# Kernel optimization log

Hardware: AMD Instinct MI355X
Metric: run time of the kernel (lower is better)

## Reference

```python
import jax, jax.numpy as jnp
import numpy as np
from jax import lax

H = 64           # hid_size (hard-pinned by reshape(4,6,64) in source)
B = 16384        # number of months (prototype batch)
A = 16           # agent_num
N = B * A        # rows of `inputs`
P = 24           # num_prototypes = 4 * 6
T = 32           # jieqi_info sequence length
ACT = 12         # action_dim
EPS = 1e-4       # self.epsilon
BN_EPS = 1e-5
LN_EPS = 1e-5


def _lstm_step(h, c, x, w_ih, w_hh, b_ih, b_hh):
    # torch LSTM gate order: i, f, g, o
    g = x @ w_ih.T + h @ w_hh.T + b_ih + b_hh
    i, f, gg, o = jnp.split(g, 4, axis=-1)
    c = jax.nn.sigmoid(f) * c + jax.nn.sigmoid(i) * jnp.tanh(gg)
    h = jax.nn.sigmoid(o) * jnp.tanh(c)
    return h, c


def setup_inputs() -> dict:
    key = jax.random.key(0)
    ks = iter(jax.random.split(key, 40))

    def nrm(shape, s=0.05):
        return jax.random.normal(next(ks), shape, jnp.float32) * s

    inp = {
        "inputs": jax.random.normal(next(ks), (N, H), jnp.float32),
        "hidden_state": jax.random.normal(next(ks), (N, H), jnp.float32),
        "month": jax.random.randint(next(ks), (B,), 0, 12, jnp.int32),
        "jieqi_info": jax.random.normal(next(ks), (P, T, 3), jnp.float32),
        # bidirectional LSTM (input 3 -> hidden H), forward + backward dirs
        "w_ih_f": nrm((4 * H, 3)), "w_hh_f": nrm((4 * H, H)),
        "b_ih_f": nrm((4 * H,)), "b_hh_f": nrm((4 * H,)),
        "w_ih_b": nrm((4 * H, 3)), "w_hh_b": nrm((4 * H, H)),
        "b_ih_b": nrm((4 * H,)), "b_hh_b": nrm((4 * H,)),
        "fcl_w": nrm((H, 2 * H)), "fcl_b": nrm((H,)),      # jieqi_lstm_fc
        "proj_w": nrm((H, H)),                               # proto_proj (no bias)
        "conv_w": nrm((H, 2 * H)), "conv_b": nrm((H,)),    # conv_global
        "bn_g": jnp.ones((H,), jnp.float32), "bn_b": jnp.zeros((H,), jnp.float32),
        "fc1_w": nrm((H, H)), "fc1_b": nrm((H,)),
        "ln_g": jnp.ones((H,), jnp.float32), "ln_b": jnp.zeros((H,), jnp.float32),
        "gru_wih": nrm((3 * H, H)), "gru_whh": nrm((3 * H, H)),
        "gru_bih": nrm((3 * H,)), "gru_bhh": nrm((3 * H,)),
        "out_w": nrm((ACT, H)), "out_b": nrm((ACT,)),
    }
    # last_layer weight: +1 on correct class, -0.5 on incorrect (set_last_layer_incorrect_connection)
    ident = np.zeros((P, 4), np.float32)
    ident[np.arange(P), np.arange(P) // 6] = 1.0
    inp["last_w"] = jnp.asarray(1.0 * ident.T + (-0.5) * (1.0 - ident.T))  # [4, 24]
    return inp


def reference(inputs, hidden_state, month, jieqi_info,
              w_ih_f, w_hh_f, b_ih_f, b_hh_f,
              w_ih_b, w_hh_b, b_ih_b, b_hh_b,
              fcl_w, fcl_b, proj_w, last_w,
              conv_w, conv_b, bn_g, bn_b,
              fc1_w, fc1_b, ln_g, ln_b,
              gru_wih, gru_whh, gru_bih, gru_bhh,
              out_w, out_b):
    dt = inputs.dtype
    # ---- get_jieqi_prototype: biLSTM over [P, T, 3], take output at t=T-1 ----
    z0 = jnp.zeros((P, H), dt)

    def step(carry, x_t):
        h, c = carry
        h, c = _lstm_step(h, c, x_t, w_ih_f, w_hh_f, b_ih_f, b_hh_f)
        return (h, c), None

    (h_f, _), _ = lax.scan(step, (z0, z0), jnp.swapaxes(jieqi_info, 0, 1))
    # backward direction's output at the last time index = one step on x[:, -1]
    h_b, _ = _lstm_step(z0, z0, jieqi_info[:, -1, :], w_ih_b, w_hh_b, b_ih_b, b_hh_b)
    th = jnp.concatenate([h_f, h_b], axis=-1)                 # [P, 2H]
    pv = jax.nn.relu(th @ fcl_w.T + fcl_b) @ proj_w.T         # prototype_vectors [P, H]

    # ---- prototype_distances on full input batch ----
    xp = inputs @ pv.T                                        # [N, P]
    min_distances = (-2.0 * xp
                     + jnp.sum(inputs ** 2, axis=1, keepdims=True)
                     + jnp.sum(pv ** 2, axis=1)[None, :])
    prototype_activations = jnp.log((min_distances + 1.0) / (min_distances + EPS))
    logits = prototype_activations @ last_w.T                 # [N, 4]

    # ---- month -> season, select seasonal prototype block ----
    seasons = jnp.mod(jnp.floor_divide(month - 2, 3), 4)      # 2-4:0, 5-7:1, 8-10:2, else 3
    sub_proto = pv.reshape(4, 6, H)[seasons]                  # [B, 6, H]

    # ---- prototype_subgraph_distances (vectorized over the 6 protos) ----
    xr = inputs.reshape(B, A, H)
    d = jnp.sum((xr[:, None, :, :] - sub_proto[:, :, None, :]) ** 2, axis=-1)  # [B, 6, A]
    sim = jnp.mean(jnp.log((d + 1.0) / (d + EPS)), axis=2)    # [B, 6]

    # ---- argmax + gather + repeat ----
    chosen_idx = jnp.argmax(sim, axis=1)                      # [B]
    chosen = sub_proto[jnp.arange(B), chosen_idx]             # [B, H]
    chosen = jnp.broadcast_to(chosen[:, None, :], (B, A, H)).reshape(N, H)

    # ---- conv_global -> batchnorm(train) -> relu ----
    x_glb = jnp.concatenate([inputs, chosen], axis=-1) @ conv_w.T + conv_b
    mu = jnp.mean(x_glb, axis=0)
    var = jnp.mean((x_glb - mu) ** 2, axis=0)                 # biased, training-mode BN
    x_glb = (x_glb - mu) * lax.rsqrt(var + BN_EPS) * bn_g + bn_b
    x_glb = jax.nn.relu(x_glb)

    # ---- fc1 -> layernorm -> relu ----
    x = x_glb @ fc1_w.T + fc1_b
    lmu = jnp.mean(x, axis=-1, keepdims=True)
    lvar = jnp.mean((x - lmu) ** 2, axis=-1, keepdims=True)
    x = (x - lmu) * lax.rsqrt(lvar + LN_EPS) * ln_g + ln_b
    x = jax.nn.relu(x)

    # ---- GRUCell ----
    h_in = hidden_state.reshape(-1, H)
    gi = x @ gru_wih.T + gru_bih
    gh = h_in @ gru_whh.T + gru_bhh
    r = jax.nn.sigmoid(gi[:, :H] + gh[:, :H])
    zg = jax.nn.sigmoid(gi[:, H:2 * H] + gh[:, H:2 * H])
    n = jnp.tanh(gi[:, 2 * H:] + r * gh[:, 2 * H:])
    h = (1.0 - zg) * n + zg * h_in

    a = h @ out_w.T + out_b
    return (a, h, logits, min_distances)
```

## Files before the change

kernel.cpp:

```cpp
#include <hip/hip_runtime.h>
#include <cmath>

#define NHID 64
#define NMONTH 16384
#define NAGENT 16
#define NROWS (NMONTH*NAGENT)
#define NPROTO 24
#define TSEQ 32
#define NACT 12
#define EPS_P  1e-4f
#define EPS_BN 1e-5f
#define EPS_LN 1e-5f

typedef __attribute__((ext_vector_type(8))) short short8;
typedef __attribute__((ext_vector_type(4))) float f32x4;
typedef __attribute__((ext_vector_type(4))) unsigned short us4;
typedef __attribute__((ext_vector_type(8))) unsigned short us8;
typedef unsigned short ushort_t;

#define MFMA(a,b,c) __builtin_amdgcn_mfma_f32_16x16x32_bf16(a,b,c,0,0,0)
#define LPAD 68

#define WS_TH     0
#define WS_PV     3072
#define WS_PVSQ   4608
#define WS_CTAB   4640
#define WS_MID1   6176
#define WS_MID2   14368
#define WS_BNSC   22560
#define WS_BNSH   22624
#define WS_WBF16  22688
#define WO_FC1   0
#define WO_GIH   4096
#define WO_GHH   16384
#define WO_OUT   28672
#define WO_PV    29696
#define WO_CVX   31744

__device__ __forceinline__ float sigf(float x){ return 1.0f/(1.0f+expf(-x)); }
__device__ __forceinline__ float fsig(float x){
  return __builtin_amdgcn_rcpf(1.f + __expf(-x));
}
__device__ __forceinline__ float ftanh(float x){
  return 1.f - 2.f*__builtin_amdgcn_rcpf(1.f + __expf(2.f*x));
}
__device__ __forceinline__ ushort_t f2bf(float f){
  unsigned u = __builtin_bit_cast(unsigned, f);
  u += 0x7FFFu + ((u>>16)&1u);
  return (ushort_t)(u>>16);
}
__device__ __forceinline__ float bf2f(ushort_t b){
  return __builtin_bit_cast(float, ((unsigned)b)<<16);
}

__global__ __launch_bounds__(256) void k1_lstm(
    const float* __restrict__ jq,
    const float* __restrict__ wif, const float* __restrict__ whf,
    const float* __restrict__ bif, const float* __restrict__ bhf,
    const float* __restrict__ wib, const float* __restrict__ bib, const float* __restrict__ bhb,
    float* __restrict__ th)
{
  const int p = blockIdx.x;
  const int j = threadIdx.x;
  __shared__ float hs[NHID];
  __shared__ float gs[4*NHID];
  float wh[NHID];
  #pragma unroll
  for (int k=0;k<NHID;k++) wh[k] = whf[j*NHID+k];
  const float wi0=wif[j*3], wi1=wif[j*3+1], wi2=wif[j*3+2];
  const float bj = bif[j]+bhf[j];
  float c = 0.f;
  if (j < NHID) hs[j] = 0.f;
  __syncthreads();
  for (int t=0;t<TSEQ;t++){
    const float x0=jq[(p*TSEQ+t)*3], x1=jq[(p*TSEQ+t)*3+1], x2=jq[(p*TSEQ+t)*3+2];
    float g = wi0*x0+wi1*x1+wi2*x2+bj;
    #pragma unroll
    for (int k=0;k<NHID;k++) g += wh[k]*hs[k];
    __syncthreads();
    gs[j] = g;
    __syncthreads();
    if (j < NHID){
      const float gi=gs[j], gf=gs[NHID+j], gg=gs[2*NHID+j], go=gs[3*NHID+j];
      c = sigf(gf)*c + sigf(gi)*tanhf(gg);
      hs[j] = sigf(go)*tanhf(c);
    }
    __syncthreads();
  }
  if (j < NHID) th[p*2*NHID + j] = hs[j];
  const float x0=jq[(p*TSEQ+TSEQ-1)*3], x1=jq[(p*TSEQ+TSEQ-1)*3+1], x2=jq[(p*TSEQ+TSEQ-1)*3+2];
  const float gb = wib[j*3]*x0 + wib[j*3+1]*x1 + wib[j*3+2]*x2 + bib[j]+bhb[j];
  __syncthreads();
  gs[j] = gb;
  __syncthreads();
  if (j < NHID){
    const float gi=gs[j], gg=gs[2*NHID+j], go=gs[3*NHID+j];
    const float cb = sigf(gi)*tanhf(gg);
    th[p*2*NHID + NHID + j] = sigf(go)*tanhf(cb);
  }
}

__global__ __launch_bounds__(64) void k2_proto(
    const float* __restrict__ th, const float* __restrict__ fclw, const float* __restrict__ fclb,
    const float* __restrict__ projw, const float* __restrict__ convw, const float* __restrict__ convb,
    float* __restrict__ pv, float* __restrict__ pvsq, float* __restrict__ ctab)
{
  const int p = blockIdx.x, h = threadIdx.x;
  __shared__ float thr[2*NHID], t1[NHID], pvr[NHID];
  thr[h]      = th[p*2*NHID+h];
  thr[NHID+h] = th[p*2*NHID+NHID+h];
  __syncthreads();
  float acc = fclb[h];
  for (int k=0;k<2*NHID;k++) acc += thr[k]*fclw[h*2*NHID+k];
  t1[h] = fmaxf(acc,0.f);
  __syncthreads();
  float pvh = 0.f;
  for (int k=0;k<NHID;k++) pvh += t1[k]*projw[h*NHID+k];
  pv[p*NHID+h]=pvh; pvr[h]=pvh;
  __syncthreads();
  float ct = convb[h];
  for (int k=0;k<NHID;k++) ct += pvr[k]*convw[h*2*NHID+NHID+k];
  ctab[p*NHID+h]=ct;
  if (h==0){ float s=0.f; for (int k=0;k<NHID;k++) s+=pvr[k]*pvr[k]; pvsq[p]=s; }
}

__global__ __launch_bounds__(256) void k5w_bf16(
    const float* __restrict__ fc1w, const float* __restrict__ gwih,
    const float* __restrict__ gwhh, const float* __restrict__ outw,
    const float* __restrict__ pvf, const float* __restrict__ convw,
    ushort_t* __restrict__ wb)
{
  const int t = threadIdx.x;
  for (int i=t;i<4096;i+=256)  wb[WO_FC1+i]=f2bf(fc1w[i]);
  for (int i=t;i<12288;i+=256){ wb[WO_GIH+i]=f2bf(gwih[i]); wb[WO_GHH+i]=f2bf(gwhh[i]); }
  for (int i=t;i<1024;i+=256)  wb[WO_OUT+i] = (i<768)? f2bf(outw[i]) : (ushort_t)0;
  for (int i=t;i<2048;i+=256)  wb[WO_PV+i]  = (i<1536)? f2bf(pvf[i]) : (ushort_t)0;
  for (int i=t;i<4096;i+=256)  wb[WO_CVX+i] = f2bf(convw[(i>>6)*128 + (i&63)]);
}

__global__ __launch_bounds__(256) void k3_mfma(
    const float* __restrict__ inp, const int* __restrict__ month,
    const float* __restrict__ pvsq, const float* __restrict__ ctab,
    const float* __restrict__ lastw, const ushort_t* __restrict__ wb,
    float* __restrict__ out_logits, float* __restrict__ out_md,
    ushort_t* __restrict__ xgb, float* __restrict__ part1, float* __restrict__ part2)
{
  __shared__ ushort_t xl[64*72];
  __shared__ float insql[64];
  __shared__ float pal[64*26];
  __shared__ int qs[4];

  const int t = threadIdx.x;
  const int w = t>>6, lane = t&63;
  const int l15 = lane&15, kg = lane>>4, ko = kg*8;
  const int gcol = w*16 + l15;
  const size_t rowblk = (size_t)blockIdx.x*64;

  const short8 pv0a = *reinterpret_cast<const short8*>(wb + WO_PV + l15*64 + ko);
  const short8 pv0b = *reinterpret_cast<const short8*>(wb + WO_PV + l15*64 + 32 + ko);
  const short8 pv1a = *reinterpret_cast<const short8*>(wb + WO_PV + (16+l15)*64 + ko);
  const short8 pv1b = *reinterpret_cast<const short8*>(wb + WO_PV + (16+l15)*64 + 32 + ko);
  const short8 cw0  = *reinterpret_cast<const short8*>(wb + WO_CVX + gcol*64 + ko);
  const short8 cw1  = *reinterpret_cast<const short8*>(wb + WO_CVX + gcol*64 + 32 + ko);

  {
    const int r = t>>2, cb = (t&3)*16;
    const float* xrow = inp + (rowblk + r)*64 + cb;
    float s = 0.f;
    #pragma unroll
    for (int i=0;i<4;i++){
      const float4 xv = *reinterpret_cast<const float4*>(xrow + i*4);
      s += xv.x*xv.x + xv.y*xv.y + xv.z*xv.z + xv.w*xv.w;
      us4 y; y.x=f2bf(xv.x); y.y=f2bf(xv.y); y.z=f2bf(xv.z); y.w=f2bf(xv.w);
      *reinterpret_cast<us4*>(&xl[r*72+cb+i*4]) = y;
    }
    s += __shfl_xor(s,1,4);
    s += __shfl_xor(s,2,4);
    if ((t&3)==0) insql[r] = s;
  }
  __syncthreads();

  const int rowA = w*16 + l15;
  const short8 ax0 = *reinterpret_cast<const short8*>(&xl[rowA*72+ko]);
  const short8 ax1 = *reinterpret_cast<const short8*>(&xl[rowA*72+32+ko]);

  f32x4 d0={0.f,0.f,0.f,0.f}, d1=d0;
  d0 = MFMA(ax0, pv0a, d0);
  d0 = MFMA(ax1, pv0b, d0);
  d1 = MFMA(ax0, pv1a, d1);
  d1 = MFMA(ax1, pv1b, d1);
  {
    const float pq0 = pvsq[l15];
    const float pq1 = (l15<8)? pvsq[16+l15] : 0.f;
    #pragma unroll
    for (int j=0;j<4;j++){
      const int rloc = w*16 + kg*4 + j;
      const float iq = insql[rloc];
      const float md0 = iq + pq0 - 2.f*d0[j];
      out_md[(rowblk+rloc)*24 + l15] = md0;
      pal[rloc*26 + l15] = __logf(md0+1.f) - __logf(md0+EPS_P);
      const float md1 = iq + pq1 - 2.f*d1[j];
      const float pa1 = __logf(md1+1.f) - __logf(md1+EPS_P);
      if (l15<8){
        out_md[(rowblk+rloc)*24 + 16+l15] = md1;
        pal[rloc*26 + 16+l15] = pa1;
      }
    }
  }
  __syncthreads();

  {
    const int r = t>>2, c = t&3;
    float lgv = 0.f;
    #pragma unroll
    for (int p=0;p<24;p++) lgv += pal[r*26+p]*lastw[c*24+p];
    out_logits[(rowblk+r)*4 + c] = lgv;
  }

  {
    const int mo = month[blockIdx.x*4 + w];
    const int season = ((mo+10)%12)/3;
    float simv = -3.4e38f;
    const int j6 = lane & 7;
    if (j6 < 6){
      simv = 0.f;
      const int sp = season*6 + j6;
      #pragma unroll
      for (int i=0;i<16;i++) simv += pal[(w*16+i)*26 + sp];
    }
    int bidx = j6;
    { const float ov=__shfl_xor(simv,1,8); const int oi=__shfl_xor(bidx,1,8);
      if (ov>simv || (ov==simv && oi<bidx)){ simv=ov; bidx=oi; } }
    { const float ov=__shfl_xor(simv,2,8); const int oi=__shfl_xor(bidx,2,8);
      if (ov>simv || (ov==simv && oi<bidx)){ simv=ov; bidx=oi; } }
    { const float ov=__shfl_xor(simv,4,8); const int oi=__shfl_xor(bidx,4,8);
      if (ov>simv || (ov==simv && oi<bidx)){ simv=ov; bidx=oi; } }
    if (lane==0) qs[w] = season*6 + bidx;
  }
  __syncthreads();

  ushort_t* xgblk = xgb + (size_t)blockIdx.x*8192;
  float s1=0.f, s2=0.f;
  #pragma unroll
  for (int rg=0; rg<4; rg++){
    const int ra = rg*16 + l15;
    const short8 bx0 = *reinterpret_cast<const short8*>(&xl[ra*72+ko]);
    const short8 bx1 = *reinterpret_cast<const short8*>(&xl[ra*72+32+ko]);
    f32x4 ac={0.f,0.f,0.f,0.f};
    ac = MFMA(bx0, cw0, ac);
    ac = MFMA(bx1, cw1, ac);
    const float cg = ctab[qs[rg]*64 + gcol];
    #pragma unroll
    for (int j=0;j<4;j++){
      const int rloc = rg*16 + kg*4 + j;
      const float v = ac[j] + cg;
      xgblk[rloc*64 + gcol] = f2bf(v);
      s1 += v; s2 += v*v;
    }
  }
  s1 += __shfl_xor(s1,16); s1 += __shfl_xor(s1,32);
  s2 += __shfl_xor(s2,16); s2 += __shfl_xor(s2,32);
  if (kg==0){
    part1[blockIdx.x*64 + gcol] = s1;
    part2[blockIdx.x*64 + gcol] = s2;
  }
}

__global__ __launch_bounds__(64) void k4b_reduce(
    const float* __restrict__ part1, const float* __restrict__ part2,
    double* __restrict__ mid1, double* __restrict__ mid2)
{
  const int i = blockIdx.x, c = threadIdx.x;
  double s1=0.0, s2=0.0;
  for (int b=i*64; b<i*64+64; b++){
    s1 += (double)part1[b*64+c];
    s2 += (double)part2[b*64+c];
  }
  mid1[i*64+c]=s1; mid2[i*64+c]=s2;
}

__global__ __launch_bounds__(64) void k5_finalize(
    const double* __restrict__ mid1, const double* __restrict__ mid2,
    const float* __restrict__ bng, const float* __restrict__ bnb,
    float* __restrict__ bnsc, float* __restrict__ bnsh)
{
  const int f = threadIdx.x;
  double s1=0.0, s2=0.0;
  for (int i=0;i<64;i++){ s1+=mid1[i*64+f]; s2+=mid2[i*64+f]; }
  const double mu = s1 / (double)NROWS;
  double var = s2/(double)NROWS - mu*mu;
  if (var < 0.0) var = 0.0;
  const float sc = bng[f] * (float)(1.0/sqrt(var + (double)EPS_BN));
  bnsc[f]=sc;
  bnsh[f]=bnb[f]-(float)mu*sc;
}

__global__ __launch_bounds__(256) void k6_mfma(
    const ushort_t* __restrict__ xgb, const float* __restrict__ hidden,
    const float* __restrict__ bnsc, const float* __restrict__ bnsh,
    const float* __restrict__ fc1b, const float* __restrict__ lng, const float* __restrict__ lnb,
    const float* __restrict__ gbih, const float* __restrict__ gbhh,
    const float* __restrict__ outb,
    const ushort_t* __restrict__ wb,
    float* __restrict__ out_a, float* __restrict__ out_h)
{
  __shared__ ushort_t ybuf[64*LPAD];
  __shared__ ushort_t hidl[64*LPAD];
  const int t = threadIdx.x;
  const int lane = t & 63, w = t >> 6;
  const int l15 = lane & 15, kg = lane >> 4;
  const int ko = kg*8;

  const short8 f0a = *reinterpret_cast<const short8*>(wb + WO_FC1 + ( 0+l15)*64 + ko);
  const short8 f0b = *reinterpret_cast<const short8*>(wb + WO_FC1 + ( 0+l15)*64 + 32 + ko);
  const short8 f1a = *reinterpret_cast<const short8*>(wb + WO_FC1 + (16+l15)*64 + ko);
  const short8 f1b = *reinterpret_cast<const short8*>(wb + WO_FC1 + (16+l15)*64 + 32 + ko);
  const short8 f2a = *reinterpret_cast<const short8*>(wb + WO_FC1 + (32+l15)*64 + ko);
  const short8 f2b = *reinterpret_cast<const short8*>(wb + WO_FC1 + (32+l15)*64 + 32 + ko);
  const short8 f3a = *reinterpret_cast<const short8*>(wb + WO_FC1 + (48+l15)*64 + ko);
  const short8 f3b = *reinterpret_cast<const short8*>(wb + WO_FC1 + (48+l15)*64 + 32 + ko);

  {
    const int r = t>>2, cb = (t&3)*16;
    const ushort_t* xgp = xgb + (size_t)blockIdx.x*8192 + r*64 + cb;
    const us8 xv0 = *reinterpret_cast<const us8*>(xgp);
    const us8 xv1 = *reinterpret_cast<const us8*>(xgp+8);
    float xf[16];
    #pragma unroll
    for (int e=0;e<8;e++){ xf[e]=bf2f(xv0[e]); xf[8+e]=bf2f(xv1[e]); }
    const size_t g = ((size_t)blockIdx.x*64 + r)*64 + cb;
    #pragma unroll
    for (int i=0;i<4;i++){
      const float4 sc = *reinterpret_cast<const float4*>(bnsc + cb + i*4);
      const float4 sh = *reinterpret_cast<const float4*>(bnsh + cb + i*4);
      us4 y;
      y.x = f2bf(fmaxf(xf[4*i  ]*sc.x+sh.x,0.f));
      y.y = f2bf(fmaxf(xf[4*i+1]*sc.y+sh.y,0.f));
      y.z = f2bf(fmaxf(xf[4*i+2]*sc.z+sh.z,0.f));
      y.w = f2bf(fmaxf(xf[4*i+3]*sc.w+sh.w,0.f));
      *reinterpret_cast<us4*>(&ybuf[r*LPAD + cb + i*4]) = y;
      const float4 hv4 = *reinterpret_cast<const float4*>(hidden + g + i*4);
      us4 hb;
      hb.x=f2bf(hv4.x); hb.y=f2bf(hv4.y); hb.z=f2bf(hv4.z); hb.w=f2bf(hv4.w);
      *reinterpret_cast<us4*>(&hidl[r*LPAD + cb + i*4]) = hb;
    }
  }
  __syncthreads();

  const int rowA = w*16 + l15;
  const short8 ay0 = *reinterpret_cast<const short8*>(&ybuf[rowA*LPAD + ko]);
  const short8 ay1 = *reinterpret_cast<const short8*>(&ybuf[rowA*LPAD + 32 + ko]);

  f32x4 ac0={0.f,0.f,0.f,0.f}, ac1=ac0, ac2=ac0, ac3=ac0;
  ac0 = MFMA(ay0, f0a, ac0);  ac0 = MFMA(ay1, f0b, ac0);
  ac1 = MFMA(ay0, f1a, ac1);  ac1 = MFMA(ay1, f1b, ac1);
  ac2 = MFMA(ay0, f2a, ac2);  ac2 = MFMA(ay1, f2b, ac2);
  ac3 = MFMA(ay0, f3a, ac3);  ac3 = MFMA(ay1, f3b, ac3);
  {
    const float b0=fc1b[l15], b1=fc1b[16+l15], b2=fc1b[32+l15], b3=fc1b[48+l15];
    float tn0[4], tn1[4], tn2[4], tn3[4], mu[4], rs[4];
    #pragma unroll
    for (int j=0;j<4;j++){ tn0[j]=ac0[j]+b0; tn1[j]=ac1[j]+b1; tn2[j]=ac2[j]+b2; tn3[j]=ac3[j]+b3; }
    #pragma unroll
    for (int j=0;j<4;j++){
      float s = tn0[j]+tn1[j]+tn2[j]+tn3[j];
      s += __shfl_xor(s,1,16); s += __shfl_xor(s,2,16);
      s += __shfl_xor(s,4,16); s += __shfl_xor(s,8,16);
      mu[j] = s*(1.f/64.f);
    }
    #pragma unroll
    for (int j=0;j<4;j++){
      const float d0_=tn0[j]-mu[j], d1_=tn1[j]-mu[j], d2_=tn2[j]-mu[j], d3_=tn3[j]-mu[j];
      float v = d0_*d0_+d1_*d1_+d2_*d2_+d3_*d3_;
      v += __shfl_xor(v,1,16); v += __shfl_xor(v,2,16);
      v += __shfl_xor(v,4,16); v += __shfl_xor(v,8,16);
      rs[j] = 1.f/sqrtf(v*(1.f/64.f)+EPS_LN);
    }
    const float g0=lng[l15], g1=lng[16+l15], g2=lng[32+l15], g3=lng[48+l15];
    const float q0=lnb[l15], q1=lnb[16+l15], q2=lnb[32+l15], q3=lnb[48+l15];
    #pragma unroll
    for (int j=0;j<4;j++){
      const int rr_ = w*16 + kg*4 + j;
      ybuf[rr_*LPAD +      l15] = f2bf(fmaxf((tn0[j]-mu[j])*rs[j]*g0+q0, 0.f));
      ybuf[rr_*LPAD + 16 + l15] = f2bf(fmaxf((tn1[j]-mu[j])*rs[j]*g1+q1, 0.f));
      ybuf[rr_*LPAD + 32 + l15] = f2bf(fmaxf((tn2[j]-mu[j])*rs[j]*g2+q2, 0.f));
      ybuf[rr_*LPAD + 48 + l15] = f2bf(fmaxf((tn3[j]-mu[j])*rs[j]*g3+q3, 0.f));
    }
  }

  const int gcol = w*16 + l15;
  const ushort_t* gih = wb + WO_GIH;
  const ushort_t* ghh = wb + WO_GHH;
  const short8 wr0 = *reinterpret_cast<const short8*>(gih + (      gcol)*64 + ko);
  const short8 wr1 = *reinterpret_cast<const short8*>(gih + (      gcol)*64 + 32 + ko);
  const short8 wz0 = *reinterpret_cast<const short8*>(gih + ( 64 + gcol)*64 + ko);
  const short8 wz1 = *reinterpret_cast<const short8*>(gih + ( 64 + gcol)*64 + 32 + ko);
  const short8 wn0 = *reinterpret_cast<const short8*>(gih + (128 + gcol)*64 + ko);
  const short8 wn1 = *reinterpret_cast<const short8*>(gih + (128 + gcol)*64 + 32 + ko);
  const short8 vr0 = *reinterpret_cast<const short8*>(ghh + (      gcol)*64 + ko);
  const short8 vr1 = *reinterpret_cast<const short8*>(ghh + (      gcol)*64 + 32 + ko);
  const short8 vz0 = *reinterpret_cast<const short8*>(ghh + ( 64 + gcol)*64 + ko);
  const short8 vz1 = *reinterpret_cast<const short8*>(ghh + ( 64 + gcol)*64 + 32 + ko);
  const short8 vn0 = *reinterpret_cast<const short8*>(ghh + (128 + gcol)*64 + ko);
  const short8 vn1 = *reinterpret_cast<const short8*>(ghh + (128 + gcol)*64 + 32 + ko);
  const float bir=gbih[gcol],     bhr=gbhh[gcol];
  const float biz=gbih[64+gcol],  bhz=gbhh[64+gcol];
  const float bin_=gbih[128+gcol],bhn=gbhh[128+gcol];
  __syncthreads();

  us4 hkeep[4];
  #pragma unroll
  for (int rg=0; rg<4; rg++){
    const int ra = rg*16 + l15;
    const short8 at0 = *reinterpret_cast<const short8*>(&ybuf[ra*LPAD + ko]);
    const short8 at1 = *reinterpret_cast<const short8*>(&ybuf[ra*LPAD + 32 + ko]);
    const short8 bh0 = *reinterpret_cast<const short8*>(&hidl[ra*LPAD + ko]);
    const short8 bh1 = *reinterpret_cast<const short8*>(&hidl[ra*LPAD + 32 + ko]);
    f32x4 ar={0.f,0.f,0.f,0.f}, az=ar, an=ar, hn=ar;
    ar = MFMA(at0, wr0, ar);  ar = MFMA(at1, wr1, ar);
    ar = MFMA(bh0, vr0, ar);  ar = MFMA(bh1, vr1, ar);
    az = MFMA(at0, wz0, az);  az = MFMA(at1, wz1, az);
    az = MFMA(bh0, vz0, az);  az = MFMA(bh1, vz1, az);
    an = MFMA(at0, wn0, an);  an = MFMA(at1, wn1, an);
    hn = MFMA(bh0, vn0, hn);  hn = MFMA(bh1, vn1, hn);
    us4 hb4;
    #pragma unroll
    for (int j=0;j<4;j++){
      const int rloc = rg*16 + kg*4 + j;
      const size_t rg_ = (size_t)blockIdx.x*64 + rloc;
      const float rrg = fsig(ar[j]+bir+bhr);
      const float zzg = fsig(az[j]+biz+bhz);
      const float nng = ftanh(an[j]+bin_ + rrg*(hn[j]+bhn));
      const float hold = bf2f(hidl[rloc*LPAD + gcol]);
      const float hv = (1.f-zzg)*nng + zzg*hold;
      out_h[rg_*64 + gcol] = hv;
      hb4[j] = f2bf(hv);
    }
    hkeep[rg] = hb4;
  }

  const short8 ow0 = *reinterpret_cast<const short8*>(wb + WO_OUT + l15*64 + ko);
  const short8 ow1 = *reinterpret_cast<const short8*>(wb + WO_OUT + l15*64 + 32 + ko);
  const float ob = (l15 < 12) ? outb[l15] : 0.f;

  __syncthreads();
  #pragma unroll
  for (int rg=0; rg<4; rg++){
    #pragma unroll
    for (int j=0;j<4;j++)
      ybuf[(rg*16 + kg*4 + j)*LPAD + gcol] = hkeep[rg][j];
  }
  __syncthreads();

  const short8 av0 = *reinterpret_cast<const short8*>(&ybuf[rowA*LPAD + ko]);
  const short8 av1 = *reinterpret_cast<const short8*>(&ybuf[rowA*LPAD + 32 + ko]);
  f32x4 aa={0.f,0.f,0.f,0.f};
  aa = MFMA(av0, ow0, aa);
  aa = MFMA(av1, ow1, aa);
  if (l15 < 12){
    #pragma unroll
    for (int j=0;j<4;j++){
      const size_t rg_ = (size_t)blockIdx.x*64 + w*16 + kg*4 + j;
      out_a[rg_*12 + l15] = aa[j] + ob;
    }
  }
}

extern "C" void kernel_launch(void* const* d_in, const int* in_sizes, int n_in,
                              void* d_out, int out_size, void* d_ws, size_t ws_size,
                              hipStream_t stream)
{
  (void)in_sizes; (void)n_in; (void)out_size; (void)ws_size;
  const float* inputs = (const float*)d_in[0];
  const float* hidden = (const float*)d_in[1];
  const int*   month  = (const int*)d_in[2];
  const float* jq     = (const float*)d_in[3];
  const float* wif    = (const float*)d_in[4];
  const float* whf    = (const float*)d_in[5];
  const float* bif    = (const float*)d_in[6];
  const float* bhf    = (const float*)d_in[7];
  const float* wib    = (const float*)d_in[8];
  const float* bib    = (const float*)d_in[10];
  const float* bhb    = (const float*)d_in[11];
  const float* fclw   = (const float*)d_in[12];
  const float* fclb   = (const float*)d_in[13];
  const float* projw  = (const float*)d_in[14];
  const float* convw  = (const float*)d_in[15];
  const float* convb  = (const float*)d_in[16];
  const float* bng    = (const float*)d_in[17];
  const float* bnb    = (const float*)d_in[18];
  const float* fc1w   = (const float*)d_in[19];
  const float* fc1b   = (const float*)d_in[20];
  const float* lng    = (const float*)d_in[21];
  const float* lnb    = (const float*)d_in[22];
  const float* gwih   = (const float*)d_in[23];
  const float* gwhh   = (const float*)d_in[24];
  const float* gbih   = (const float*)d_in[25];
  const float* gbhh   = (const float*)d_in[26];
  const float* outw   = (const float*)d_in[27];
  const float* outb   = (const float*)d_in[28];
  const float* lastw  = (const float*)d_in[29];

  float* ws  = (float*)d_ws;
  float* out = (float*)d_out;
  float* out_a  = out;
  float* out_h  = out + (size_t)NROWS*NACT;
  float* out_lg = out + (size_t)NROWS*(NACT+NHID);
  float* out_md = out + (size_t)NROWS*(NACT+NHID+4);
  ushort_t* wb = (ushort_t*)(ws + WS_WBF16);
  ushort_t* xgb = (ushort_t*)out_h;
  float* part1 = out_a;
  float* part2 = out_a + 4096*64;

  hipLaunchKernelGGL(k1_lstm, dim3(NPROTO), dim3(256), 0, stream,
                     jq, wif, whf, bif, bhf, wib, bib, bhb, ws+WS_TH);
  hipLaunchKernelGGL(k2_proto, dim3(NPROTO), dim3(64), 0, stream,
                     ws+WS_TH, fclw, fclb, projw, convw, convb,
                     ws+WS_PV, ws+WS_PVSQ, ws+WS_CTAB);
  hipLaunchKernelGGL(k5w_bf16, dim3(1), dim3(256), 0, stream,
                     fc1w, gwih, gwhh, outw, ws+WS_PV, convw, wb);
  hipLaunchKernelGGL(k3_mfma, dim3(NROWS/64), dim3(256), 0, stream,
                     inputs, month, ws+WS_PVSQ, ws+WS_CTAB, lastw, wb,
                     out_lg, out_md, xgb, part1, part2);
  hipLaunchKernelGGL(k4b_reduce, dim3(64), dim3(64), 0, stream,
                     part1, part2, (double*)(ws+WS_MID1), (double*)(ws+WS_MID2));
  hipLaunchKernelGGL(k5_finalize, dim3(1), dim3(64), 0, stream,
                     (const double*)(ws+WS_MID1), (const double*)(ws+WS_MID2),
                     bng, bnb, ws+WS_BNSC, ws+WS_BNSH);
  hipLaunchKernelGGL(k6_mfma, dim3(NROWS/64), dim3(256), 0, stream,
                     xgb, hidden, ws+WS_BNSC, ws+WS_BNSH, fc1b, lng, lnb,
                     gbih, gbhh, outb, wb, out_a, out_h);
}
```

Measured before the change: 161.1 us.

## Make each wave own its rows to replace block barriers with wave-local fences

In k3_mfma and k6_mfma the work split changes so each wave owns 16 rows across all 64 output columns, instead of 16 columns across all 64 rows. Because every value a wave reads from shared memory is now written by that same wave, the block-wide __syncthreads calls become an LDS waitcnt fence, and the qs shared array and the hkeep staging for the output matmul go away. The cost is that the conv and GRU weight fragments are loaded inside the per-column-tile loop, roughly four times more weight loads per wave. The BN partial sums are also written per wave, four times as many, so k4b_reduce reads four times more partials and their offsets grow accordingly.

```diff
diff --git a/kernel.cpp b/kernel.cpp
--- a/kernel.cpp
+++ b/kernel.cpp
@@ -20,6 +20,7 @@
 
 #define MFMA(a,b,c) __builtin_amdgcn_mfma_f32_16x16x32_bf16(a,b,c,0,0,0)
 #define LPAD 68
+#define LDSFENCE() asm volatile("s_waitcnt lgkmcnt(0)" ::: "memory")
 
 #define WS_TH     0
 #define WS_PV     3072
@@ -148,23 +149,22 @@
   __shared__ ushort_t xl[64*72];
   __shared__ float insql[64];
   __shared__ float pal[64*26];
-  __shared__ int qs[4];
 
   const int t = threadIdx.x;
   const int w = t>>6, lane = t&63;
   const int l15 = lane&15, kg = lane>>4, ko = kg*8;
-  const int gcol = w*16 + l15;
+  const int rbase = w*16;
   const size_t rowblk = (size_t)blockIdx.x*64;
 
   const short8 pv0a = *reinterpret_cast<const short8*>(wb + WO_PV + l15*64 + ko);
   const short8 pv0b = *reinterpret_cast<const short8*>(wb + WO_PV + l15*64 + 32 + ko);
   const short8 pv1a = *reinterpret_cast<const short8*>(wb + WO_PV + (16+l15)*64 + ko);
   const short8 pv1b = *reinterpret_cast<const short8*>(wb + WO_PV + (16+l15)*64 + 32 + ko);
-  const short8 cw0  = *reinterpret_cast<const short8*>(wb + WO_CVX + gcol*64 + ko);
-  const short8 cw1  = *reinterpret_cast<const short8*>(wb + WO_CVX + gcol*64 + 32 + ko);
+  const int mo = month[blockIdx.x*4 + w];
+  const int season = ((mo+10)%12)/3;
 
   {
-    const int r = t>>2, cb = (t&3)*16;
+    const int r = rbase + (lane>>2), cb = (lane&3)*16;
     const float* xrow = inp + (rowblk + r)*64 + cb;
     float s = 0.f;
     #pragma unroll
@@ -176,11 +176,11 @@
     }
     s += __shfl_xor(s,1,4);
     s += __shfl_xor(s,2,4);
-    if ((t&3)==0) insql[r] = s;
-  }
-  __syncthreads();
-
-  const int rowA = w*16 + l15;
+    if ((lane&3)==0) insql[r] = s;
+  }
+  LDSFENCE();
+
+  const int rowA = rbase + l15;
   const short8 ax0 = *reinterpret_cast<const short8*>(&xl[rowA*72+ko]);
   const short8 ax1 = *reinterpret_cast<const short8*>(&xl[rowA*72+32+ko]);
 
@@ -194,7 +194,7 @@
     const float pq1 = (l15<8)? pvsq[16+l15] : 0.f;
     #pragma unroll
     for (int j=0;j<4;j++){
-      const int rloc = w*16 + kg*4 + j;
+      const int rloc = rbase + kg*4 + j;
       const float iq = insql[rloc];
       const float md0 = iq + pq0 - 2.f*d0[j];
       out_md[(rowblk+rloc)*24 + l15] = md0;
@@ -207,26 +207,25 @@
       }
     }
   }
-  __syncthreads();
+  LDSFENCE();
 
   {
-    const int r = t>>2, c = t&3;
+    const int r2 = rbase + (lane>>2), c = lane&3;
     float lgv = 0.f;
     #pragma unroll
-    for (int p=0;p<24;p++) lgv += pal[r*26+p]*lastw[c*24+p];
-    out_logits[(rowblk+r)*4 + c] = lgv;
-  }
-
+    for (int p=0;p<24;p++) lgv += pal[r2*26+p]*lastw[c*24+p];
+    out_logits[(rowblk+r2)*4 + c] = lgv;
+  }
+
+  int qsw;
   {
-    const int mo = month[blockIdx.x*4 + w];
-    const int season = ((mo+10)%12)/3;
     float simv = -3.4e38f;
     const int j6 = lane & 7;
     if (j6 < 6){
       simv = 0.f;
       const int sp = season*6 + j6;
       #pragma unroll
-      for (int i=0;i<16;i++) simv += pal[(w*16+i)*26 + sp];
+      for (int i=0;i<16;i++) simv += pal[(rbase+i)*26 + sp];
     }
     int bidx = j6;
     { const float ov=__shfl_xor(simv,1,8); const int oi=__shfl_xor(bidx,1,8);
@@ -235,34 +234,33 @@
       if (ov>simv || (ov==simv && oi<bidx)){ simv=ov; bidx=oi; } }
     { const float ov=__shfl_xor(simv,4,8); const int oi=__shfl_xor(bidx,4,8);
       if (ov>simv || (ov==simv && oi<bidx)){ simv=ov; bidx=oi; } }
-    if (lane==0) qs[w] = season*6 + bidx;
-  }
-  __syncthreads();
+    qsw = season*6 + bidx;
+  }
 
   ushort_t* xgblk = xgb + (size_t)blockIdx.x*8192;
-  float s1=0.f, s2=0.f;
   #pragma unroll
-  for (int rg=0; rg<4; rg++){
-    const int ra = rg*16 + l15;
-    const short8 bx0 = *reinterpret_cast<const short8*>(&xl[ra*72+ko]);
-    const short8 bx1 = *reinterpret_cast<const short8*>(&xl[ra*72+32+ko]);
+  for (int ct=0; ct<4; ct++){
+    const int c = ct*16 + l15;
+    const short8 cw0 = *reinterpret_cast<const short8*>(wb + WO_CVX + c*64 + ko);
+    const short8 cw1 = *reinterpret_cast<const short8*>(wb + WO_CVX + c*64 + 32 + ko);
     f32x4 ac={0.f,0.f,0.f,0.f};
-    ac = MFMA(bx0, cw0, ac);
-    ac = MFMA(bx1, cw1, ac);
-    const float cg = ctab[qs[rg]*64 + gcol];
-    #pragma unroll
-    for (int j=0;j<4;j++){
-      const int rloc = rg*16 + kg*4 + j;
+    ac = MFMA(ax0, cw0, ac);
+    ac = MFMA(ax1, cw1, ac);
+    const float cg = ctab[qsw*64 + c];
+    float s1=0.f, s2=0.f;
+    #pragma unroll
+    for (int j=0;j<4;j++){
+      const int rloc = rbase + kg*4 + j;
       const float v = ac[j] + cg;
-      xgblk[rloc*64 + gcol] = f2bf(v);
+      xgblk[rloc*64 + c] = f2bf(v);
       s1 += v; s2 += v*v;
     }
-  }
-  s1 += __shfl_xor(s1,16); s1 += __shfl_xor(s1,32);
-  s2 += __shfl_xor(s2,16); s2 += __shfl_xor(s2,32);
-  if (kg==0){
-    part1[blockIdx.x*64 + gcol] = s1;
-    part2[blockIdx.x*64 + gcol] = s2;
+    s1 += __shfl_xor(s1,16); s1 += __shfl_xor(s1,32);
+    s2 += __shfl_xor(s2,16); s2 += __shfl_xor(s2,32);
+    if (kg==0){
+      part1[((size_t)blockIdx.x*4 + w)*64 + c] = s1;
+      part2[((size_t)blockIdx.x*4 + w)*64 + c] = s2;
+    }
   }
 }
 
@@ -272,7 +270,7 @@
 {
   const int i = blockIdx.x, c = threadIdx.x;
   double s1=0.0, s2=0.0;
-  for (int b=i*64; b<i*64+64; b++){
+  for (int b=i*256; b<i*256+256; b++){
     s1 += (double)part1[b*64+c];
     s2 += (double)part2[b*64+c];
   }
@@ -310,6 +308,7 @@
   const int lane = t & 63, w = t >> 6;
   const int l15 = lane & 15, kg = lane >> 4;
   const int ko = kg*8;
+  const int rbase = w*16;
 
   const short8 f0a = *reinterpret_cast<const short8*>(wb + WO_FC1 + ( 0+l15)*64 + ko);
   const short8 f0b = *reinterpret_cast<const short8*>(wb + WO_FC1 + ( 0+l15)*64 + 32 + ko);
@@ -321,7 +320,7 @@
   const short8 f3b = *reinterpret_cast<const short8*>(wb + WO_FC1 + (48+l15)*64 + 32 + ko);
 
   {
-    const int r = t>>2, cb = (t&3)*16;
+    const int r = rbase + (lane>>2), cb = (lane&3)*16;
     const ushort_t* xgp = xgb + (size_t)blockIdx.x*8192 + r*64 + cb;
     const us8 xv0 = *reinterpret_cast<const us8*>(xgp);
     const us8 xv1 = *reinterpret_cast<const us8*>(xgp+8);
@@ -345,11 +344,13 @@
       *reinterpret_cast<us4*>(&hidl[r*LPAD + cb + i*4]) = hb;
     }
   }
-  __syncthreads();
-
-  const int rowA = w*16 + l15;
+  LDSFENCE();
+
+  const int rowA = rbase + l15;
   const short8 ay0 = *reinterpret_cast<const short8*>(&ybuf[rowA*LPAD + ko]);
   const short8 ay1 = *reinterpret_cast<const short8*>(&ybuf[rowA*LPAD + 32 + ko]);
+  const short8 bh0 = *reinterpret_cast<const short8*>(&hidl[rowA*LPAD + ko]);
+  const short8 bh1 = *reinterpret_cast<const short8*>(&hidl[rowA*LPAD + 32 + ko]);
 
   f32x4 ac0={0.f,0.f,0.f,0.f}, ac1=ac0, ac2=ac0, ac3=ac0;
   ac0 = MFMA(ay0, f0a, ac0);  ac0 = MFMA(ay1, f0b, ac0);
@@ -380,42 +381,39 @@
     const float q0=lnb[l15], q1=lnb[16+l15], q2=lnb[32+l15], q3=lnb[48+l15];
     #pragma unroll
     for (int j=0;j<4;j++){
-      const int rr_ = w*16 + kg*4 + j;
+      const int rr_ = rbase + kg*4 + j;
       ybuf[rr_*LPAD +      l15] = f2bf(fmaxf((tn0[j]-mu[j])*rs[j]*g0+q0, 0.f));
       ybuf[rr_*LPAD + 16 + l15] = f2bf(fmaxf((tn1[j]-mu[j])*rs[j]*g1+q1, 0.f));
       ybuf[rr_*LPAD + 32 + l15] = f2bf(fmaxf((tn2[j]-mu[j])*rs[j]*g2+q2, 0.f));
       ybuf[rr_*LPAD + 48 + l15] = f2bf(fmaxf((tn3[j]-mu[j])*rs[j]*g3+q3, 0.f));
     }
   }
-
-  const int gcol = w*16 + l15;
+  LDSFENCE();
+
+  const short8 at0 = *reinterpret_cast<const short8*>(&ybuf[rowA*LPAD + ko]);
+  const short8 at1 = *reinterpret_cast<const short8*>(&ybuf[rowA*LPAD + 32 + ko]);
+
   const ushort_t* gih = wb + WO_GIH;
   const ushort_t* ghh = wb + WO_GHH;
-  const short8 wr0 = *reinterpret_cast<const short8*>(gih + (      gcol)*64 + ko);
-  const short8 wr1 = *reinterpret_cast<const short8*>(gih + (      gcol)*64 + 32 + ko);
-  const short8 wz0 = *reinterpret_cast<const short8*>(gih + ( 64 + gcol)*64 + ko);
-  const short8 wz1 = *reinterpret_cast<const short8*>(gih + ( 64 + gcol)*64 + 32 + ko);
-  const short8 wn0 = *reinterpret_cast<const short8*>(gih + (128 + gcol)*64 + ko);
-  const short8 wn1 = *reinterpret_cast<const short8*>(gih + (128 + gcol)*64 + 32 + ko);
-  const short8 vr0 = *reinterpret_cast<const short8*>(ghh + (      gcol)*64 + ko);
-  const short8 vr1 = *reinterpret_cast<const short8*>(ghh + (      gcol)*64 + 32 + ko);
-  const short8 vz0 = *reinterpret_cast<const short8*>(ghh + ( 64 + gcol)*64 + ko);
-  const short8 vz1 = *reinterpret_cast<const short8*>(ghh + ( 64 + gcol)*64 + 32 + ko);
-  const short8 vn0 = *reinterpret_cast<const short8*>(ghh + (128 + gcol)*64 + ko);
-  const short8 vn1 = *reinterpret_cast<const short8*>(ghh + (128 + gcol)*64 + 32 + ko);
-  const float bir=gbih[gcol],     bhr=gbhh[gcol];
-  const float biz=gbih[64+gcol],  bhz=gbhh[64+gcol];
-  const float bin_=gbih[128+gcol],bhn=gbhh[128+gcol];
-  __syncthreads();
-
-  us4 hkeep[4];
   #pragma unroll
-  for (int rg=0; rg<4; rg++){
-    const int ra = rg*16 + l15;
-    const short8 at0 = *reinterpret_cast<const short8*>(&ybuf[ra*LPAD + ko]);
-    const short8 at1 = *reinterpret_cast<const short8*>(&ybuf[ra*LPAD + 32 + ko]);
-    const short8 bh0 = *reinterpret_cast<const short8*>(&hidl[ra*LPAD + ko]);
-    const short8 bh1 = *reinterpret_cast<const short8*>(&hidl[ra*LPAD + 32 + ko]);
+  for (int ct=0; ct<4; ct++){
+    const int c = ct*16 + l15;
+    const short8 wr0 = *reinterpret_cast<const short8*>(gih + (      c)*64 + ko);
+    const short8 wr1 = *reinterpret_cast<const short8*>(gih + (      c)*64 + 32 + ko);
+    const short8 wz0 = *reinterpret_cast<const short8*>(gih + ( 64 + c)*64 + ko);
+    const short8 wz1 = *reinterpret_cast<const short8*>(gih + ( 64 + c)*64 + 32 + ko);
+    const short8 wn0 = *reinterpret_cast<const short8*>(gih + (128 + c)*64 + ko);
+    const short8 wn1 = *reinterpret_cast<const short8*>(gih + (128 + c)*64 + 32 + ko);
+    const short8 vr0 = *reinterpret_cast<const short8*>(ghh + (      c)*64 + ko);
+    const short8 vr1 = *reinterpret_cast<const short8*>(ghh + (      c)*64 + 32 + ko);
+    const short8 vz0 = *reinterpret_cast<const short8*>(ghh + ( 64 + c)*64 + ko);
+    const short8 vz1 = *reinterpret_cast<const short8*>(ghh + ( 64 + c)*64 + 32 + ko);
+    const short8 vn0 = *reinterpret_cast<const short8*>(ghh + (128 + c)*64 + ko);
+    const short8 vn1 = *reinterpret_cast<const short8*>(ghh + (128 + c)*64 + 32 + ko);
+    const float br  = gbih[c]      + gbhh[c];
+    const float bz  = gbih[64+c]   + gbhh[64+c];
+    const float bn_ = gbih[128+c];
+    const float bhn = gbhh[128+c];
     f32x4 ar={0.f,0.f,0.f,0.f}, az=ar, an=ar, hn=ar;
     ar = MFMA(at0, wr0, ar);  ar = MFMA(at1, wr1, ar);
     ar = MFMA(bh0, vr0, ar);  ar = MFMA(bh1, vr1, ar);
@@ -423,34 +421,24 @@
     az = MFMA(bh0, vz0, az);  az = MFMA(bh1, vz1, az);
     an = MFMA(at0, wn0, an);  an = MFMA(at1, wn1, an);
     hn = MFMA(bh0, vn0, hn);  hn = MFMA(bh1, vn1, hn);
-    us4 hb4;
-    #pragma unroll
-    for (int j=0;j<4;j++){
-      const int rloc = rg*16 + kg*4 + j;
+    #pragma unroll
+    for (int j=0;j<4;j++){
+      const int rloc = rbase + kg*4 + j;
       const size_t rg_ = (size_t)blockIdx.x*64 + rloc;
-      const float rrg = fsig(ar[j]+bir+bhr);
-      const float zzg = fsig(az[j]+biz+bhz);
-      const float nng = ftanh(an[j]+bin_ + rrg*(hn[j]+bhn));
-      const float hold = bf2f(hidl[rloc*LPAD + gcol]);
+      const float rrg = fsig(ar[j]+br);
+      const float zzg = fsig(az[j]+bz);
+      const float nng = ftanh(an[j]+bn_ + rrg*(hn[j]+bhn));
+      const float hold = bf2f(hidl[rloc*LPAD + c]);
       const float hv = (1.f-zzg)*nng + zzg*hold;
-      out_h[rg_*64 + gcol] = hv;
-      hb4[j] = f2bf(hv);
-    }
-    hkeep[rg] = hb4;
+      out_h[rg_*64 + c] = hv;
+      ybuf[rloc*LPAD + c] = f2bf(hv);
+    }
   }
 
   const short8 ow0 = *reinterpret_cast<const short8*>(wb + WO_OUT + l15*64 + ko);
   const short8 ow1 = *reinterpret_cast<const short8*>(wb + WO_OUT + l15*64 + 32 + ko);
   const float ob = (l15 < 12) ? outb[l15] : 0.f;
-
-  __syncthreads();
-  #pragma unroll
-  for (int rg=0; rg<4; rg++){
-    #pragma unroll
-    for (int j=0;j<4;j++)
-      ybuf[(rg*16 + kg*4 + j)*LPAD + gcol] = hkeep[rg][j];
-  }
-  __syncthreads();
+  LDSFENCE();
 
   const short8 av0 = *reinterpret_cast<const short8*>(&ybuf[rowA*LPAD + ko]);
   const short8 av1 = *reinterpret_cast<const short8*>(&ybuf[rowA*LPAD + 32 + ko]);
@@ -460,7 +448,7 @@
   if (l15 < 12){
     #pragma unroll
     for (int j=0;j<4;j++){
-      const size_t rg_ = (size_t)blockIdx.x*64 + w*16 + kg*4 + j;
+      const size_t rg_ = (size_t)blockIdx.x*64 + rbase + kg*4 + j;
       out_a[rg_*12 + l15] = aa[j] + ob;
     }
   }
@@ -510,7 +498,7 @@
   ushort_t* wb = (ushort_t*)(ws + WS_WBF16);
   ushort_t* xgb = (ushort_t*)out_h;
   float* part1 = out_a;
-  float* part2 = out_a + 4096*64;
+  float* part2 = out_a + (size_t)16384*64;
 
   hipLaunchKernelGGL(k1_lstm, dim3(NPROTO), dim3(256), 0, stream,
                      jq, wif, whf, bif, bhf, wib, bib, bhb, ws+WS_TH);
```

Result: slower. 244.3 us (+51.6%).
